# Performance work log

Hardware: AMD Instinct MI355X
Metric: run time of the kernel (lower is better)

Reference implementation:

```python
import jax, jax.numpy as jnp
import numpy as np

NE, S, B, IN, H, L, NL = 16, 16, 256, 61, 1024, 512, 2


def _gru_cell(x, h, wih, whh, bih, bhh):
    # PyTorch GRUCell math, gate order (r, z, n)
    gi = x @ wih.T + bih
    gh = h @ whh.T + bhh
    i_r, i_z, i_n = jnp.split(gi, 3, axis=-1)
    h_r, h_z, h_n = jnp.split(gh, 3, axis=-1)
    r = jax.nn.sigmoid(i_r + h_r)
    z = jax.nn.sigmoid(i_z + h_z)
    n = jnp.tanh(i_n + r * h_n)
    return (1.0 - z) * n + z * h


def setup_inputs():
    key = jax.random.key(0)
    ks = jax.random.split(key, 26)
    def w(i, shape, s=0.05):
        return jax.random.normal(ks[i], shape, jnp.float32) * s
    return {
        "target": jax.random.normal(ks[0], (NE * S, B, IN), jnp.float32),
        "latent": jax.random.normal(ks[1], (B, L), jnp.float32),
        "h0": jnp.zeros((NL, B, H), jnp.float32),
        "h0_dec": jax.random.normal(ks[2], (NE, NL, B, H), jnp.float32),
        "c_wih0": w(3, (3 * H, L)), "c_whh0": w(4, (3 * H, H)),
        "c_bih0": w(5, (3 * H,)), "c_bhh0": w(6, (3 * H,)),
        "c_wih1": w(7, (3 * H, H)), "c_whh1": w(8, (3 * H, H)),
        "c_bih1": w(9, (3 * H,)), "c_bhh1": w(10, (3 * H,)),
        "ce_w": w(11, (L, H)), "ce_b": w(12, (L,)),
        "d_wih0": w(13, (3 * H, IN + L)), "d_whh0": w(14, (3 * H, H)),
        "d_bih0": w(15, (3 * H,)), "d_bhh0": w(16, (3 * H,)),
        "d_wih1": w(17, (3 * H, H)), "d_whh1": w(18, (3 * H, H)),
        "d_bih1": w(19, (3 * H,)), "d_bhh1": w(20, (3 * H,)),
        "o_w": w(21, (IN, H)), "o_b": w(22, (IN,)),
    }


def reference(target, latent, h0, h0_dec,
              c_wih0, c_whh0, c_bih0, c_bhh0,
              c_wih1, c_whh1, c_bih1, c_bhh1,
              ce_w, ce_b,
              d_wih0, d_whh0, d_bih0, d_bhh0,
              d_wih1, d_whh1, d_bih1, d_bhh1,
              o_w, o_b):
    # --- Conductor: NE single-timestep 2-layer GRU steps, same latent input each step ---
    def cond_step(h, _):
        h0n = _gru_cell(latent, h[0], c_wih0, c_whh0, c_bih0, c_bhh0)
        h1n = _gru_cell(h0n, h[1], c_wih1, c_whh1, c_bih1, c_bhh1)
        return jnp.stack([h0n, h1n]), h1n
    _, c_out = jax.lax.scan(cond_step, h0, None, length=NE)  # [NE, B, H]
    emb = jnp.tanh(c_out @ ce_w.T + ce_b)                    # [NE, B, L]

    # --- Decoder (teacher forcing): segments independent -> fold NE into batch ---
    x = target.reshape(NE, S, B, IN).transpose(1, 0, 2, 3)   # [S, NE, B, IN]
    emb_rep = jnp.broadcast_to(emb[None], (S, NE, B, L))
    e = jnp.concatenate([x, emb_rep], axis=-1).reshape(S, NE * B, IN + L)
    hd = h0_dec.transpose(1, 0, 2, 3).reshape(NL, NE * B, H)

    def dec_step(h, xt):
        h0n = _gru_cell(xt, h[0], d_wih0, d_whh0, d_bih0, d_bhh0)
        h1n = _gru_cell(h0n, h[1], d_wih1, d_whh1, d_bih1, d_bhh1)
        return jnp.stack([h0n, h1n]), h1n
    _, y = jax.lax.scan(dec_step, hd, e)                     # [S, NE*B, H]

    probs = jax.nn.softmax(y @ o_w.T + o_b, axis=-1)         # [S, NE*B, IN]
    out = probs.reshape(S, NE, B, IN).transpose(1, 0, 2, 3).reshape(NE * S, B, IN)
    return out
```

## Files before the change

kernel.cpp:

```cpp
#include <hip/hip_runtime.h>
#include <hip/hip_bf16.h>
#include <cstdint>
#include <cstddef>

#define NEc 16
#define SSc 16
#define BBc 256
#define INc 61
#define HHc 1024
#define LLc 512
#define H3c 3072
#define NEBc 4096
#define KXc 64
#define HB  16

typedef __hip_bfloat16 bf16;
typedef __attribute__((ext_vector_type(8))) short bf16x8;
typedef __attribute__((ext_vector_type(4))) float f32x4;
typedef __attribute__((ext_vector_type(4))) short s16x4;

__device__ __forceinline__ void gload16(const void* g, void* l){
    __builtin_amdgcn_global_load_lds((const __attribute__((address_space(1))) unsigned int*)g,
                                     (__attribute__((address_space(3))) unsigned int*)l, 16, 0, 0);
}

__device__ __forceinline__ float sigmoidf_(float x){ return 1.0f/(1.0f+__expf(-x)); }

struct Slice {
    const bf16* A0; int lda0; int K0;
    const bf16* A1; int lda1; int K1;
    const bf16* A2; int lda2;
    const bf16* Wlo;
    const bf16* Whi;
    const float* bp;
    const float* hin;
    float* hout;
    bf16* hbout;
    bf16* out2;
    int mode;
};

#define GRU_KSTEP(APTR, ALDA, ACOL, BPTR, BLDB, BCOL, NIDX)                              \
  {                                                                                      \
    if (!first) __syncthreads();                                                         \
    first = false;                                                                       \
    _Pragma("unroll")                                                                    \
    for (int i=0;i<MR;i++){                                                              \
        const int o = i*4096 + tid*16;                                                   \
        const int u = o ^ (((o>>7)&7)<<4);                                               \
        gload16((APTR) + (size_t)(m0 + (u>>7))*(ALDA) + (ACOL) + ((u&127)>>1), sA + o);  \
    }                                                                                    \
    _Pragma("unroll")                                                                    \
    for (int i=0;i<6;i++){                                                               \
        const int o = i*4096 + tid*16;                                                   \
        const int u = o ^ (((o>>7)&7)<<4);                                               \
        gload16((BPTR) + (size_t)(u>>7)*(BLDB) + (BCOL) + ((u&127)>>1), sB + o);         \
    }                                                                                    \
    __syncthreads();                                                                     \
    _Pragma("unroll")                                                                    \
    for (int ks=0;ks<2;ks++){                                                            \
        bf16x8 av[MR];                                                                   \
        _Pragma("unroll")                                                                \
        for (int mi=0;mi<MR;mi++){                                                       \
            const int r = wm*(BM/2) + mi*16 + lr;                                        \
            const int u = r*128 + ks*64 + lk*16;                                         \
            av[mi] = *(const bf16x8*)(sA + (u ^ ((r&7)<<4)));                            \
        }                                                                                \
        _Pragma("unroll")                                                                \
        for (int hs=0;hs<2;hs++){                                                        \
            _Pragma("unroll")                                                            \
            for (int g3=0;g3<3;g3++){                                                    \
                const int br = ((wc*2+hs)*3 + g3)*16 + lr;                               \
                const int u  = br*128 + ks*64 + lk*16;                                   \
                const bf16x8 bv = *(const bf16x8*)(sB + (u ^ ((br&7)<<4)));              \
                const int gi_ = (g3<2) ? g3 : (NIDX);                                    \
                _Pragma("unroll")                                                        \
                for (int mi=0;mi<MR;mi++)                                                \
                    acc[mi][hs][gi_] = __builtin_amdgcn_mfma_f32_16x16x32_bf16(          \
                        av[mi], bv, acc[mi][hs][gi_], 0,0,0);                            \
            }                                                                            \
        }                                                                                \
    }                                                                                    \
  }

template<int BM>
__device__ void gru_body(const Slice& s, char* smem)
{
    constexpr int MR = BM/32;
    char* sA = smem;
    char* sB = smem + BM*128;

    const int tid  = threadIdx.x;
    const int lane = tid & 63;
    const int wave = tid >> 6;
    const int wm   = wave >> 1;
    const int wc   = wave & 1;
    const int lr   = lane & 15;
    const int lk   = lane >> 4;
    const int hb   = blockIdx.y;
    const int m0   = blockIdx.x * BM;

    const int Klo = s.K0 + s.K1;
    const bf16* WloB = s.Wlo + (size_t)hb*192*Klo;
    const bf16* WhiB = s.Whi + (size_t)hb*192*1024;

    f32x4 acc[MR][2][4];
    #pragma unroll
    for (int mi=0;mi<MR;mi++)
      #pragma unroll
      for (int hs=0;hs<2;hs++)
        #pragma unroll
        for (int g=0;g<4;g++)
          #pragma unroll
          for (int j=0;j<4;j++) acc[mi][hs][g][j] = 0.f;

    float hpre[2][MR][4];
    #pragma unroll
    for (int hs=0;hs<2;hs++)
      #pragma unroll
      for (int mi=0;mi<MR;mi++)
        #pragma unroll
        for (int j=0;j<4;j++){
            const int rl = wm*(BM/2) + mi*16 + lk*4 + j;
            hpre[hs][mi][j] = s.hin[(size_t)(m0+rl)*HHc + hb*64 + (wc*2+hs)*16 + lr];
        }

    bool first = true;

    {
        const bf16* Ap = s.A0; const int Al = s.lda0; const int Kp = s.K0;
        for (int k0 = 0; k0 < Kp; k0 += 64) GRU_KSTEP(Ap, Al, k0, WloB, Klo, k0, 2)
    }
    if (s.K1 > 0){
        const bf16* Ap = s.A1; const int Al = s.lda1; const int Kp = s.K1; const int c0 = s.K0;
        for (int k0 = 0; k0 < Kp; k0 += 64) GRU_KSTEP(Ap, Al, k0, WloB, Klo, c0 + k0, 2)
    }
    {
        const bf16* Ap = s.A2; const int Al = s.lda2;
        for (int k0 = 0; k0 < 1024; k0 += 64) GRU_KSTEP(Ap, Al, k0, WhiB, 1024, k0, 3)
    }

    #pragma unroll
    for (int hs=0;hs<2;hs++){
        const int hsub = wc*2 + hs;
        const int hc   = hb*64 + hsub*16 + lr;
        const float bpr  = s.bp[hb*256 +       hsub*16 + lr];
        const float bpz  = s.bp[hb*256 +  64 + hsub*16 + lr];
        const float bpin = s.bp[hb*256 + 128 + hsub*16 + lr];
        const float bphn = s.bp[hb*256 + 192 + hsub*16 + lr];
        #pragma unroll
        for (int mi=0;mi<MR;mi++)
          #pragma unroll
          for (int j=0;j<4;j++){
            const int rl = wm*(BM/2) + mi*16 + lk*4 + j;
            const int m  = m0 + rl;
            const float r = sigmoidf_(acc[mi][hs][0][j] + bpr);
            const float z = sigmoidf_(acc[mi][hs][1][j] + bpz);
            const float n = tanhf(acc[mi][hs][2][j] + bpin + r*(acc[mi][hs][3][j] + bphn));
            const size_t off = (size_t)m*HHc + hc;
            const float hnew = (1.f - z)*n + z*hpre[hs][mi][j];
            s.hout[off] = hnew;
            const bf16 hb16 = __float2bfloat16(hnew);
            s.hbout[off] = hb16;
            if (s.out2) s.out2[off] = hb16;
          }
    }
}

__device__ void owsm_body(const Slice& s, char* smem)
{
    if (blockIdx.y != 0) return;
    char* sA = smem; char* sB = smem + 8192;
    const int tid  = threadIdx.x;
    const int lane = tid & 63;
    const int wave = tid >> 6;
    const int wm   = wave >> 1;
    const int wc   = wave & 1;
    const int lr   = lane & 15;
    const int lk   = lane >> 4;
    const int m0   = blockIdx.x * 64;
    const int t    = s.K0;

    f32x4 acc[2][2];
    #pragma unroll
    for (int mi=0;mi<2;mi++)
      #pragma unroll
      for (int ni=0;ni<2;ni++)
        #pragma unroll
        for (int j=0;j<4;j++) acc[mi][ni][j]=0.f;

    for (int k0=0;k0<1024;k0+=64){
        if (k0) __syncthreads();
        #pragma unroll
        for (int i=0;i<2;i++){
            const int o = i*4096 + tid*16;
            const int u = o ^ (((o>>7)&7)<<4);
            gload16(s.A0 + (size_t)(m0 + (u>>7))*1024 + k0 + ((u&127)>>1), sA + o);
        }
        #pragma unroll
        for (int i=0;i<2;i++){
            const int o = i*4096 + tid*16;
            const int u = o ^ (((o>>7)&7)<<4);
            gload16(s.Wlo + (size_t)(u>>7)*1024 + k0 + ((u&127)>>1), sB + o);
        }
        __syncthreads();
        #pragma unroll
        for (int ks=0;ks<2;ks++){
            bf16x8 av[2], bv[2];
            #pragma unroll
            for (int mi=0;mi<2;mi++){
                const int r = wm*32 + mi*16 + lr;
                const int u = r*128 + ks*64 + lk*16;
                av[mi] = *(const bf16x8*)(sA + (u ^ ((r&7)<<4)));
            }
            #pragma unroll
            for (int ni=0;ni<2;ni++){
                const int r = wc*32 + ni*16 + lr;
                const int u = r*128 + ks*64 + lk*16;
                bv[ni] = *(const bf16x8*)(sB + (u ^ ((r&7)<<4)));
            }
            #pragma unroll
            for (int mi=0;mi<2;mi++)
              #pragma unroll
              for (int ni=0;ni<2;ni++)
                acc[mi][ni] = __builtin_amdgcn_mfma_f32_16x16x32_bf16(av[mi], bv[ni], acc[mi][ni], 0,0,0);
        }
    }
    __syncthreads();
    float* lg = (float*)smem;
    #pragma unroll
    for (int mi=0;mi<2;mi++)
      #pragma unroll
      for (int ni=0;ni<2;ni++)
        #pragma unroll
        for (int j=0;j<4;j++){
            const int rl = wm*32 + mi*16 + lk*4 + j;
            const int c  = wc*32 + ni*16 + lr;
            lg[rl*68 + c] = (c < INc) ? (acc[mi][ni][j] + s.bp[c]) : -1e30f;
        }
    __syncthreads();
    const int row = tid >> 2;
    const int q   = tid & 3;
    float mx = -1e30f;
    #pragma unroll
    for (int i=0;i<16;i++) mx = fmaxf(mx, lg[row*68 + q*16+i]);
    mx = fmaxf(mx, __shfl_xor(mx,1));
    mx = fmaxf(mx, __shfl_xor(mx,2));
    float ev[16];
    float sum = 0.f;
    #pragma unroll
    for (int i=0;i<16;i++){ ev[i] = __expf(lg[row*68 + q*16+i] - mx); sum += ev[i]; }
    sum += __shfl_xor(sum,1);
    sum += __shfl_xor(sum,2);
    const float inv = 1.f/sum;
    const int R = m0 + row;
    const int ne = R >> 8, b = R & 255;
    float* op = s.hout + ((size_t)((ne*SSc + t)*BBc + b))*INc;
    #pragma unroll
    for (int i=0;i<16;i++){
        const int c = q*16 + i;
        if (c < INc) op[c] = ev[i]*inv;
    }
}

template<int BM>
__global__ __launch_bounds__(256)
void fused_step(Slice s0, Slice s1, Slice s2)
{
    __shared__ char smem[(BM+192)*128];
    const Slice& s = (blockIdx.z==0) ? s0 : (blockIdx.z==1) ? s1 : s2;
    if (s.mode < 0) return;
    if constexpr (BM>=64){
        if (s.mode == 1){ owsm_body(s, smem); return; }
    }
    gru_body<BM>(s, smem);
}

template<int BM,int BN>
__global__ __launch_bounds__(256)
void gemm_bf(const bf16* __restrict__ A, const bf16* __restrict__ Bm, float* __restrict__ C,
             int K, int ldc)
{
    constexpr int WAVES_M = (BM==128) ? 2 : 1;
    constexpr int WM = BM / WAVES_M;
    constexpr int WN = BN / (4/WAVES_M);
    constexpr int MR = WM / 16;
    constexpr int NR = WN / 16;
    constexpr int ASW = (BM*128)/4096;
    constexpr int BSW = (BN*128)/4096;

    __shared__ char smem[(BM+BN)*128];
    char* sA = smem;
    char* sB = smem + BM*128;

    const int tid  = threadIdx.x;
    const int lane = tid & 63;
    const int wave = tid >> 6;
    const int wm   = (WAVES_M==2) ? (wave>>1) : 0;
    const int wn   = (WAVES_M==2) ? (wave&1)  : wave;
    const int lr   = lane & 15;
    const int lk   = lane >> 4;
    const int m0   = blockIdx.y * BM;
    const int n0   = blockIdx.x * BN;

    f32x4 acc[MR][NR];
    #pragma unroll
    for (int mi=0;mi<MR;mi++)
      #pragma unroll
      for (int ni=0;ni<NR;ni++)
        #pragma unroll
        for (int j=0;j<4;j++) acc[mi][ni][j] = 0.f;

    for (int k0 = 0; k0 < K; k0 += 64){
        if (k0) __syncthreads();
        #pragma unroll
        for (int i=0;i<ASW;i++){
            const int o = i*4096 + tid*16;
            const int u = o ^ (((o>>7)&7)<<4);
            gload16(A + (size_t)(m0 + (u>>7))*K + k0 + ((u&127)>>1), sA + o);
        }
        #pragma unroll
        for (int i=0;i<BSW;i++){
            const int o = i*4096 + tid*16;
            const int u = o ^ (((o>>7)&7)<<4);
            gload16(Bm + (size_t)(n0 + (u>>7))*K + k0 + ((u&127)>>1), sB + o);
        }
        __syncthreads();
        #pragma unroll
        for (int ks=0;ks<2;ks++){
            bf16x8 av[MR], bv[NR];
            #pragma unroll
            for (int mi=0;mi<MR;mi++){
                const int r = wm*WM + mi*16 + lr;
                const int u = r*128 + ks*64 + lk*16;
                av[mi] = *(const bf16x8*)(sA + (u ^ ((r&7)<<4)));
            }
            #pragma unroll
            for (int ni=0;ni<NR;ni++){
                const int r = wn*WN + ni*16 + lr;
                const int u = r*128 + ks*64 + lk*16;
                bv[ni] = *(const bf16x8*)(sB + (u ^ ((r&7)<<4)));
            }
            #pragma unroll
            for (int mi=0;mi<MR;mi++)
              #pragma unroll
              for (int ni=0;ni<NR;ni++)
                acc[mi][ni] = __builtin_amdgcn_mfma_f32_16x16x32_bf16(av[mi], bv[ni], acc[mi][ni], 0,0,0);
        }
    }
    #pragma unroll
    for (int mi=0;mi<MR;mi++)
      #pragma unroll
      for (int ni=0;ni<NR;ni++)
        #pragma unroll
        for (int j=0;j<4;j++){
            const int r = m0 + wm*WM + mi*16 + lk*4 + j;
            const int c = n0 + wn*WN + ni*16 + lr;
            C[(size_t)r*ldc + c] = acc[mi][ni][j];
        }
}

__global__ __launch_bounds__(256) void pack_w2(const float* __restrict__ src, int srcld,
                                               int col0, int Kvalid, int Kchunk,
                                               bf16* __restrict__ dst, int dstld, int dstc0,
                                               int total){
    const int idx = blockIdx.x*256 + threadIdx.x;
    if (idx >= total) return;
    const int k  = idx % Kchunk;
    const int c  = (idx / Kchunk) % 192;
    const int hb = idx / (Kchunk*192);
    const int g  = c >> 4;
    const int hsub = g/3;
    const int gate = g - hsub*3;
    const int row = gate*HHc + hb*64 + hsub*16 + (c & 15);
    const float v = (k < Kvalid) ? src[(size_t)row*srcld + col0 + k] : 0.f;
    dst[((size_t)hb*192 + c)*dstld + dstc0 + k] = __float2bfloat16(v);
}

__global__ __launch_bounds__(256) void pack_bias(const float* __restrict__ bih,
                                                 const float* __restrict__ bhh,
                                                 float* __restrict__ bp){
    const int idx = blockIdx.x*256 + threadIdx.x;
    if (idx >= HB*256) return;
    const int c  = idx & 255;
    const int hb = idx >> 8;
    const int i  = hb*64 + (c&63);
    const int g  = c >> 6;
    float v;
    if      (g==0) v = bih[i] + bhh[i];
    else if (g==1) v = bih[HHc+i] + bhh[HHc+i];
    else if (g==2) v = bih[2*HHc+i];
    else           v = bhh[2*HHc+i];
    bp[idx] = v;
}

__global__ __launch_bounds__(256) void cvt_bf16_k(const float* __restrict__ in, bf16* __restrict__ out, int n4){
    const int i = blockIdx.x*256 + threadIdx.x;
    if (i >= n4) return;
    const f32x4 v = *(const f32x4*)(in + (size_t)i*4);
    union { s16x4 s; bf16 b[4]; } u;
    #pragma unroll
    for (int j=0;j<4;j++) u.b[j] = __float2bfloat16(v[j]);
    *(s16x4*)(out + (size_t)i*4) = u.s;
}

__global__ __launch_bounds__(256) void pad_ow(const float* __restrict__ w, bf16* __restrict__ o){
    const int idx = blockIdx.x*256 + threadIdx.x;
    if (idx >= KXc*HHc) return;
    const int r = idx >> 10;
    o[idx] = __float2bfloat16(r < INc ? w[(size_t)r*HHc + (idx & (HHc-1))] : 0.f);
}

__global__ __launch_bounds__(256) void build_xb(const float* __restrict__ t, bf16* __restrict__ xb){
    const int idx = blockIdx.x*256 + threadIdx.x;
    if (idx >= SSc*NEBc*KXc) return;
    const int c  = idx & 63;
    const int rr = idx >> 6;
    const int s  = rr >> 12;
    const int r  = rr & 4095;
    const int ne = r >> 8;
    const int b  = r & 255;
    const float v = (c < INc) ? t[(((size_t)(ne*SSc + s)*BBc + b)*INc) + c] : 0.f;
    xb[idx] = __float2bfloat16(v);
}

__global__ __launch_bounds__(256) void init_hc(const float* __restrict__ h0,
                                               float* __restrict__ h0c, float* __restrict__ h1c,
                                               bf16* __restrict__ h0cb, bf16* __restrict__ h1cb){
    const int i = blockIdx.x*256 + threadIdx.x;
    if (i >= (BBc*HHc)/4) return;
    const int e = i*4;
    f32x4 a = *(const f32x4*)(h0 + e);
    f32x4 b = *(const f32x4*)(h0 + BBc*HHc + e);
    union { s16x4 v; bf16 q[4]; } ua, ub;
    #pragma unroll
    for (int j=0;j<4;j++){ ua.q[j]=__float2bfloat16(a[j]); ub.q[j]=__float2bfloat16(b[j]); }
    *(f32x4*)(h0c + e) = a; *(f32x4*)(h1c + e) = b;
    *(s16x4*)(h0cb + e) = ua.v; *(s16x4*)(h1cb + e) = ub.v;
}

__global__ __launch_bounds__(256) void init_hd(const float* __restrict__ hd,
                                               float* __restrict__ hd0, float* __restrict__ hd1,
                                               bf16* __restrict__ hd0b, bf16* __restrict__ hd1b){
    const int i = blockIdx.x*256 + threadIdx.x;
    if (i >= (NEBc*HHc)/4) return;
    const int e  = i*4;
    const int hh = e & (HHc-1);
    const int r  = e >> 10;
    const int ne = r >> 8;
    const int b  = r & 255;
    f32x4 a = *(const f32x4*)(hd + (((size_t)ne*2 + 0)*BBc + b)*HHc + hh);
    f32x4 c = *(const f32x4*)(hd + (((size_t)ne*2 + 1)*BBc + b)*HHc + hh);
    union { s16x4 v; bf16 q[4]; } ua, uc;
    #pragma unroll
    for (int j=0;j<4;j++){ ua.q[j]=__float2bfloat16(a[j]); uc.q[j]=__float2bfloat16(c[j]); }
    *(f32x4*)(hd0 + e) = a; *(f32x4*)(hd1 + e) = c;
    *(s16x4*)(hd0b + e) = ua.v; *(s16x4*)(hd1b + e) = uc.v;
}

__global__ __launch_bounds__(256) void bias_tanh4(const float* __restrict__ in,
                                                  const float* __restrict__ b, bf16* __restrict__ out){
    const int i = blockIdx.x*256 + threadIdx.x;
    if (i >= (NEBc*LLc)/4) return;
    const int e = i*4;
    const int c = e & (LLc-1);
    f32x4 v = *(const f32x4*)(in + e);
    f32x4 bb = *(const f32x4*)(b + c);
    union { s16x4 s; bf16 q[4]; } u;
    #pragma unroll
    for (int j=0;j<4;j++) u.q[j] = __float2bfloat16(tanhf(v[j] + bb[j]));
    *(s16x4*)(out + e) = u.s;
}


extern "C" void kernel_launch(void* const* d_in, const int* in_sizes, int n_in,
                              void* d_out, int out_size, void* d_ws, size_t ws_size,
                              hipStream_t stream)
{
    const float* target = (const float*)d_in[0];
    const float* latent = (const float*)d_in[1];
    const float* h0     = (const float*)d_in[2];
    const float* h0_dec = (const float*)d_in[3];
    const float* c_wih0 = (const float*)d_in[4];
    const float* c_whh0 = (const float*)d_in[5];
    const float* c_bih0 = (const float*)d_in[6];
    const float* c_bhh0 = (const float*)d_in[7];
    const float* c_wih1 = (const float*)d_in[8];
    const float* c_whh1 = (const float*)d_in[9];
    const float* c_bih1 = (const float*)d_in[10];
    const float* c_bhh1 = (const float*)d_in[11];
    const float* ce_w   = (const float*)d_in[12];
    const float* ce_b   = (const float*)d_in[13];
    const float* d_wih0 = (const float*)d_in[14];
    const float* d_whh0 = (const float*)d_in[15];
    const float* d_bih0 = (const float*)d_in[16];
    const float* d_bhh0 = (const float*)d_in[17];
    const float* d_wih1 = (const float*)d_in[18];
    const float* d_whh1 = (const float*)d_in[19];
    const float* d_bih1 = (const float*)d_in[20];
    const float* d_bhh1 = (const float*)d_in[21];
    const float* o_w    = (const float*)d_in[22];
    const float* o_b    = (const float*)d_in[23];
    float* out = (float*)d_out;

    float* fp = (float*)d_ws;
    auto fa = [&](size_t n){ float* q = fp; fp += n; return q; };
    float* hd0f[2] = { fa((size_t)NEBc*HHc), fa((size_t)NEBc*HHc) };
    float* hd1f[2] = { fa((size_t)NEBc*HHc), fa((size_t)NEBc*HHc) };
    float* h0cf[2] = { fa((size_t)BBc*HHc),  fa((size_t)BBc*HHc) };
    float* h1cf[2] = { fa((size_t)BBc*HHc),  fa((size_t)BBc*HHc) };
    float* emb   = fa((size_t)NEBc*LLc);
    float* bp_c0 = fa(HB*256);
    float* bp_c1 = fa(HB*256);
    float* bp_d0 = fa(HB*256);
    float* bp_d1 = fa(HB*256);

    bf16* bbp = (bf16*)fp;
    auto ba = [&](size_t n){ bf16* q = bbp; bbp += n; return q; };
    bf16* hd0b[2] = { ba((size_t)NEBc*HHc), ba((size_t)NEBc*HHc) };
    bf16* hd1b[2] = { ba((size_t)NEBc*HHc), ba((size_t)NEBc*HHc) };
    bf16* h0cb[2] = { ba((size_t)BBc*HHc),  ba((size_t)BBc*HHc) };
    bf16* h1cb[2] = { ba((size_t)BBc*HHc),  ba((size_t)BBc*HHc) };
    bf16* xb     = ba((size_t)SSc*NEBc*KXc);
    bf16* coutb  = ba((size_t)NEBc*HHc);
    bf16* embb   = ba((size_t)NEBc*LLc);
    bf16* latb   = ba((size_t)BBc*LLc);
    bf16* Wloc0  = ba((size_t)HB*192*LLc);
    bf16* Whic0  = ba((size_t)HB*192*HHc);
    bf16* Wloc1  = ba((size_t)HB*192*HHc);
    bf16* Whic1  = ba((size_t)HB*192*HHc);
    bf16* Wlod0f = ba((size_t)HB*192*576);
    bf16* Whid0  = ba((size_t)HB*192*HHc);
    bf16* Wlod1  = ba((size_t)HB*192*HHc);
    bf16* Whid1  = ba((size_t)HB*192*HHc);
    bf16* cewb   = ba((size_t)LLc*HHc);
    bf16* owb    = ba((size_t)KXc*HHc);

    auto packw = [&](const float* src, int srcld, int col0, int kv, int kchunk,
                     bf16* dst, int dstld, int dstc0){
        const int tot = HB*192*kchunk;
        hipLaunchKernelGGL(pack_w2, dim3((tot+255)/256), dim3(256),0,stream,
                           src,srcld,col0,kv,kchunk,dst,dstld,dstc0,tot);
    };

    hipLaunchKernelGGL(cvt_bf16_k, dim3((BBc*LLc/4+255)/256), dim3(256),0,stream, latent, latb, BBc*LLc/4);
    hipLaunchKernelGGL(cvt_bf16_k, dim3((LLc*HHc/4+255)/256), dim3(256),0,stream, ce_w, cewb, LLc*HHc/4);
    hipLaunchKernelGGL(pad_ow, dim3((KXc*HHc)/256), dim3(256),0,stream, o_w, owb);
    hipLaunchKernelGGL(build_xb, dim3((SSc*NEBc*KXc)/256), dim3(256),0,stream, target, xb);
    hipLaunchKernelGGL(init_hc, dim3((BBc*HHc/4)/256), dim3(256),0,stream, h0, h0cf[0], h1cf[0], h0cb[0], h1cb[0]);
    hipLaunchKernelGGL(init_hd, dim3((NEBc*HHc/4)/256), dim3(256),0,stream, h0_dec, hd0f[0], hd1f[0], hd0b[0], hd1b[0]);
    packw(c_wih0, LLc,     0,   LLc, LLc,  Wloc0, LLc, 0);
    packw(c_whh0, HHc,     0,   HHc, HHc,  Whic0, HHc, 0);
    packw(c_wih1, HHc,     0,   HHc, HHc,  Wloc1, HHc, 0);
    packw(c_whh1, HHc,     0,   HHc, HHc,  Whic1, HHc, 0);
    packw(d_wih0, INc+LLc, 0,   INc, KXc,  Wlod0f, 576, 0);
    packw(d_wih0, INc+LLc, INc, LLc, LLc,  Wlod0f, 576, KXc);
    packw(d_whh0, HHc,     0,   HHc, HHc,  Whid0, HHc, 0);
    packw(d_wih1, HHc,     0,   HHc, HHc,  Wlod1, HHc, 0);
    packw(d_whh1, HHc,     0,   HHc, HHc,  Whid1, HHc, 0);
    hipLaunchKernelGGL(pack_bias, dim3((HB*256+255)/256), dim3(256),0,stream, c_bih0, c_bhh0, bp_c0);
    hipLaunchKernelGGL(pack_bias, dim3((HB*256+255)/256), dim3(256),0,stream, c_bih1, c_bhh1, bp_c1);
    hipLaunchKernelGGL(pack_bias, dim3((HB*256+255)/256), dim3(256),0,stream, d_bih0, d_bhh0, bp_d0);
    hipLaunchKernelGGL(pack_bias, dim3((HB*256+255)/256), dim3(256),0,stream, d_bih1, d_bhh1, bp_d1);

    auto CL0 = [&](int s){ Slice x{}; x.mode=0;
        x.A0=latb; x.lda0=LLc; x.K0=LLc; x.A1=nullptr; x.lda1=0; x.K1=0;
        x.A2=h0cb[s&1]; x.lda2=HHc; x.Wlo=Wloc0; x.Whi=Whic0; x.bp=bp_c0;
        x.hin=h0cf[s&1]; x.hout=h0cf[(s+1)&1]; x.hbout=h0cb[(s+1)&1]; x.out2=nullptr; return x; };
    auto CL1 = [&](int s){ Slice x{}; x.mode=0;
        x.A0=h0cb[(s+1)&1]; x.lda0=HHc; x.K0=HHc; x.A1=nullptr; x.lda1=0; x.K1=0;
        x.A2=h1cb[s&1]; x.lda2=HHc; x.Wlo=Wloc1; x.Whi=Whic1; x.bp=bp_c1;
        x.hin=h1cf[s&1]; x.hout=h1cf[(s+1)&1]; x.hbout=h1cb[(s+1)&1];
        x.out2=coutb + (size_t)s*BBc*HHc; return x; };
    auto DL0 = [&](int t){ Slice x{}; x.mode=0;
        x.A0=xb + (size_t)t*NEBc*KXc; x.lda0=KXc; x.K0=KXc;
        x.A1=embb; x.lda1=LLc; x.K1=LLc;
        x.A2=hd0b[t&1]; x.lda2=HHc; x.Wlo=Wlod0f; x.Whi=Whid0; x.bp=bp_d0;
        x.hin=hd0f[t&1]; x.hout=hd0f[(t+1)&1]; x.hbout=hd0b[(t+1)&1]; x.out2=nullptr; return x; };
    auto DL1 = [&](int t){ Slice x{}; x.mode=0;
        x.A0=hd0b[(t+1)&1]; x.lda0=HHc; x.K0=HHc; x.A1=nullptr; x.lda1=0; x.K1=0;
        x.A2=hd1b[t&1]; x.lda2=HHc; x.Wlo=Wlod1; x.Whi=Whid1; x.bp=bp_d1;
        x.hin=hd1f[t&1]; x.hout=hd1f[(t+1)&1]; x.hbout=hd1b[(t+1)&1]; x.out2=nullptr; return x; };
    auto OW = [&](int t){ Slice x{}; x.mode=1;
        x.A0=hd1b[(t+1)&1]; x.K0=t; x.Wlo=owb; x.bp=o_b; x.hout=out; return x; };
    Slice NS{}; NS.mode = -1;

    hipLaunchKernelGGL((fused_step<32>), dim3(BBc/32, HB, 1), dim3(256),0,stream, CL0(0), NS, NS);
    for (int s=0;s<NEc;s++){
        if (s < NEc-1)
            hipLaunchKernelGGL((fused_step<32>), dim3(BBc/32, HB, 2), dim3(256),0,stream,
                               CL1(s), CL0(s+1), NS);
        else
            hipLaunchKernelGGL((fused_step<32>), dim3(BBc/32, HB, 1), dim3(256),0,stream,
                               CL1(s), NS, NS);
    }

    hipLaunchKernelGGL((gemm_bf<64,128>), dim3(LLc/128, NEBc/64), dim3(256),0,stream,
                       coutb, cewb, emb, HHc, LLc);
    hipLaunchKernelGGL(bias_tanh4, dim3((NEBc*LLc/4)/256), dim3(256),0,stream, emb, ce_b, embb);

    hipLaunchKernelGGL((fused_step<64>), dim3(NEBc/64, HB, 1), dim3(256),0,stream, DL0(0), NS, NS);
    for (int t=0;t<SSc;t++){
        Slice s1 = (t < SSc-1) ? DL0(t+1) : NS;
        Slice s2 = (t >= 1) ? OW(t-1) : NS;
        const int nz = (t >= 1) ? 3 : 2;
        hipLaunchKernelGGL((fused_step<64>), dim3(NEBc/64, HB, nz), dim3(256),0,stream,
                           DL1(t), s1, s2);
    }
    hipLaunchKernelGGL((fused_step<64>), dim3(NEBc/64, 1, 1), dim3(256),0,stream, OW(SSc-1), NS, NS);
}
```

Measured before the change: 2.993 ms.

## Pre-pack GRU weights into MFMA fragment layout and read directly from global

Weights are repacked so each wave's B-operand fragment for a 32-wide K window is a contiguous 512-element chunk indexed by lane. The kernel now reads weights straight from global/L2 into registers instead of staging them through LDS, which shrinks shared memory and removes the B tile global-to-LDS copy per K-step. The previous-hidden preload is also dropped and re-read at the epilogue. The risk is that register-level global loads of weights stall the MFMA stream, since they are not pipelined and sit on the critical path after the barrier.

```diff
diff --git a/kernel.cpp b/kernel.cpp
--- a/kernel.cpp
+++ b/kernel.cpp
@@ -40,21 +40,15 @@
     int mode;
 };
 
-#define GRU_KSTEP(APTR, ALDA, ACOL, BPTR, BLDB, BCOL, NIDX)                              \
+#define GRU_KSTEP(APTR, ALDA, ACOL, WF, KW, NIDX)                                        \
   {                                                                                      \
     if (!first) __syncthreads();                                                         \
     first = false;                                                                       \
     _Pragma("unroll")                                                                    \
-    for (int i=0;i<MR;i++){                                                              \
+    for (int i=0;i<ASW;i++){                                                             \
         const int o = i*4096 + tid*16;                                                   \
         const int u = o ^ (((o>>7)&7)<<4);                                               \
         gload16((APTR) + (size_t)(m0 + (u>>7))*(ALDA) + (ACOL) + ((u&127)>>1), sA + o);  \
-    }                                                                                    \
-    _Pragma("unroll")                                                                    \
-    for (int i=0;i<6;i++){                                                               \
-        const int o = i*4096 + tid*16;                                                   \
-        const int u = o ^ (((o>>7)&7)<<4);                                               \
-        gload16((BPTR) + (size_t)(u>>7)*(BLDB) + (BCOL) + ((u&127)>>1), sB + o);         \
     }                                                                                    \
     __syncthreads();                                                                     \
     _Pragma("unroll")                                                                    \
@@ -66,13 +60,13 @@
             const int u = r*128 + ks*64 + lk*16;                                         \
             av[mi] = *(const bf16x8*)(sA + (u ^ ((r&7)<<4)));                            \
         }                                                                                \
+        const bf16* wp = (WF) + ((size_t)((KW)+ks)*12)*512 + (size_t)lane*8;             \
         _Pragma("unroll")                                                                \
         for (int hs=0;hs<2;hs++){                                                        \
             _Pragma("unroll")                                                            \
             for (int g3=0;g3<3;g3++){                                                    \
-                const int br = ((wc*2+hs)*3 + g3)*16 + lr;                               \
-                const int u  = br*128 + ks*64 + lk*16;                                   \
-                const bf16x8 bv = *(const bf16x8*)(sB + (u ^ ((br&7)<<4)));              \
+                const int f = (wc*2+hs)*3 + g3;                                          \
+                const bf16x8 bv = *(const bf16x8*)(wp + f*512);                          \
                 const int gi_ = (g3<2) ? g3 : (NIDX);                                    \
                 _Pragma("unroll")                                                        \
                 for (int mi=0;mi<MR;mi++)                                                \
@@ -86,9 +80,9 @@
 template<int BM>
 __device__ void gru_body(const Slice& s, char* smem)
 {
-    constexpr int MR = BM/32;
+    constexpr int MR  = BM/32;
+    constexpr int ASW = (BM*128)/4096;
     char* sA = smem;
-    char* sB = smem + BM*128;
 
     const int tid  = threadIdx.x;
     const int lane = tid & 63;
@@ -101,8 +95,8 @@
     const int m0   = blockIdx.x * BM;
 
     const int Klo = s.K0 + s.K1;
-    const bf16* WloB = s.Wlo + (size_t)hb*192*Klo;
-    const bf16* WhiB = s.Whi + (size_t)hb*192*1024;
+    const bf16* WloF = s.Wlo + (size_t)hb * ((size_t)(Klo>>5)*12*512);
+    const bf16* WhiF = s.Whi + (size_t)hb * ((size_t)32*12*512);
 
     f32x4 acc[MR][2][4];
     #pragma unroll
@@ -114,30 +108,19 @@
           #pragma unroll
           for (int j=0;j<4;j++) acc[mi][hs][g][j] = 0.f;
 
-    float hpre[2][MR][4];
-    #pragma unroll
-    for (int hs=0;hs<2;hs++)
-      #pragma unroll
-      for (int mi=0;mi<MR;mi++)
-        #pragma unroll
-        for (int j=0;j<4;j++){
-            const int rl = wm*(BM/2) + mi*16 + lk*4 + j;
-            hpre[hs][mi][j] = s.hin[(size_t)(m0+rl)*HHc + hb*64 + (wc*2+hs)*16 + lr];
-        }
-
     bool first = true;
 
     {
         const bf16* Ap = s.A0; const int Al = s.lda0; const int Kp = s.K0;
-        for (int k0 = 0; k0 < Kp; k0 += 64) GRU_KSTEP(Ap, Al, k0, WloB, Klo, k0, 2)
+        for (int k0 = 0; k0 < Kp; k0 += 64) GRU_KSTEP(Ap, Al, k0, WloF, (k0>>5), 2)
     }
     if (s.K1 > 0){
         const bf16* Ap = s.A1; const int Al = s.lda1; const int Kp = s.K1; const int c0 = s.K0;
-        for (int k0 = 0; k0 < Kp; k0 += 64) GRU_KSTEP(Ap, Al, k0, WloB, Klo, c0 + k0, 2)
+        for (int k0 = 0; k0 < Kp; k0 += 64) GRU_KSTEP(Ap, Al, k0, WloF, ((c0+k0)>>5), 2)
     }
     {
         const bf16* Ap = s.A2; const int Al = s.lda2;
-        for (int k0 = 0; k0 < 1024; k0 += 64) GRU_KSTEP(Ap, Al, k0, WhiB, 1024, k0, 3)
+        for (int k0 = 0; k0 < 1024; k0 += 64) GRU_KSTEP(Ap, Al, k0, WhiF, (k0>>5), 3)
     }
 
     #pragma unroll
@@ -158,7 +141,7 @@
             const float z = sigmoidf_(acc[mi][hs][1][j] + bpz);
             const float n = tanhf(acc[mi][hs][2][j] + bpin + r*(acc[mi][hs][3][j] + bphn));
             const size_t off = (size_t)m*HHc + hc;
-            const float hnew = (1.f - z)*n + z*hpre[hs][mi][j];
+            const float hnew = (1.f - z)*n + z*s.hin[off];
             s.hout[off] = hnew;
             const bf16 hb16 = __float2bfloat16(hnew);
             s.hbout[off] = hb16;
@@ -267,7 +250,8 @@
 __global__ __launch_bounds__(256)
 void fused_step(Slice s0, Slice s1, Slice s2)
 {
-    __shared__ char smem[(BM+192)*128];
+    constexpr int SMEMSZ = (BM >= 64) ? 17408 : BM*128;
+    __shared__ char smem[SMEMSZ];
     const Slice& s = (blockIdx.z==0) ? s0 : (blockIdx.z==1) ? s1 : s2;
     if (s.mode < 0) return;
     if constexpr (BM>=64){
@@ -360,9 +344,9 @@
         }
 }
 
-__global__ __launch_bounds__(256) void pack_w2(const float* __restrict__ src, int srcld,
+__global__ __launch_bounds__(256) void pack_w3(const float* __restrict__ src, int srcld,
                                                int col0, int Kvalid, int Kchunk,
-                                               bf16* __restrict__ dst, int dstld, int dstc0,
+                                               bf16* __restrict__ dst, int nkw, int kw0,
                                                int total){
     const int idx = blockIdx.x*256 + threadIdx.x;
     if (idx >= total) return;
@@ -372,9 +356,13 @@
     const int g  = c >> 4;
     const int hsub = g/3;
     const int gate = g - hsub*3;
-    const int row = gate*HHc + hb*64 + hsub*16 + (c & 15);
-    const float v = (k < Kvalid) ? src[(size_t)row*srcld + col0 + k] : 0.f;
-    dst[((size_t)hb*192 + c)*dstld + dstc0 + k] = __float2bfloat16(v);
+    const int srow = gate*HHc + hb*64 + hsub*16 + (c & 15);
+    const float v = (k < Kvalid) ? src[(size_t)srow*srcld + col0 + k] : 0.f;
+    const int kwin = kw0 + (k >> 5);
+    const int kl   = k & 31;
+    const int lane = (kl >> 3)*16 + (c & 15);
+    const int j    = kl & 7;
+    dst[((((size_t)hb*nkw + kwin)*12 + g)*64 + lane)*8 + j] = __float2bfloat16(v);
 }
 
 __global__ __launch_bounds__(256) void pack_bias(const float* __restrict__ bih,
@@ -537,10 +525,10 @@
     bf16* owb    = ba((size_t)KXc*HHc);
 
     auto packw = [&](const float* src, int srcld, int col0, int kv, int kchunk,
-                     bf16* dst, int dstld, int dstc0){
+                     bf16* dst, int nkw, int kw0){
         const int tot = HB*192*kchunk;
-        hipLaunchKernelGGL(pack_w2, dim3((tot+255)/256), dim3(256),0,stream,
-                           src,srcld,col0,kv,kchunk,dst,dstld,dstc0,tot);
+        hipLaunchKernelGGL(pack_w3, dim3((tot+255)/256), dim3(256),0,stream,
+                           src,srcld,col0,kv,kchunk,dst,nkw,kw0,tot);
     };
 
     hipLaunchKernelGGL(cvt_bf16_k, dim3((BBc*LLc/4+255)/256), dim3(256),0,stream, latent, latb, BBc*LLc/4);
@@ -549,15 +537,15 @@
     hipLaunchKernelGGL(build_xb, dim3((SSc*NEBc*KXc)/256), dim3(256),0,stream, target, xb);
     hipLaunchKernelGGL(init_hc, dim3((BBc*HHc/4)/256), dim3(256),0,stream, h0, h0cf[0], h1cf[0], h0cb[0], h1cb[0]);
     hipLaunchKernelGGL(init_hd, dim3((NEBc*HHc/4)/256), dim3(256),0,stream, h0_dec, hd0f[0], hd1f[0], hd0b[0], hd1b[0]);
-    packw(c_wih0, LLc,     0,   LLc, LLc,  Wloc0, LLc, 0);
-    packw(c_whh0, HHc,     0,   HHc, HHc,  Whic0, HHc, 0);
-    packw(c_wih1, HHc,     0,   HHc, HHc,  Wloc1, HHc, 0);
-    packw(c_whh1, HHc,     0,   HHc, HHc,  Whic1, HHc, 0);
-    packw(d_wih0, INc+LLc, 0,   INc, KXc,  Wlod0f, 576, 0);
-    packw(d_wih0, INc+LLc, INc, LLc, LLc,  Wlod0f, 576, KXc);
-    packw(d_whh0, HHc,     0,   HHc, HHc,  Whid0, HHc, 0);
-    packw(d_wih1, HHc,     0,   HHc, HHc,  Wlod1, HHc, 0);
-    packw(d_whh1, HHc,     0,   HHc, HHc,  Whid1, HHc, 0);
+    packw(c_wih0, LLc,     0,   LLc, LLc, Wloc0, 16, 0);
+    packw(c_whh0, HHc,     0,   HHc, HHc, Whic0, 32, 0);
+    packw(c_wih1, HHc,     0,   HHc, HHc, Wloc1, 32, 0);
+    packw(c_whh1, HHc,     0,   HHc, HHc, Whic1, 32, 0);
+    packw(d_wih0, INc+LLc, 0,   INc, KXc, Wlod0f, 18, 0);
+    packw(d_wih0, INc+LLc, INc, LLc, LLc, Wlod0f, 18, 2);
+    packw(d_whh0, HHc,     0,   HHc, HHc, Whid0, 32, 0);
+    packw(d_wih1, HHc,     0,   HHc, HHc, Wlod1, 32, 0);
+    packw(d_whh1, HHc,     0,   HHc, HHc, Whid1, 32, 0);
     hipLaunchKernelGGL(pack_bias, dim3((HB*256+255)/256), dim3(256),0,stream, c_bih0, c_bhh0, bp_c0);
     hipLaunchKernelGGL(pack_bias, dim3((HB*256+255)/256), dim3(256),0,stream, c_bih1, c_bhh1, bp_c1);
     hipLaunchKernelGGL(pack_bias, dim3((HB*256+255)/256), dim3(256),0,stream, d_bih0, d_bhh0, bp_d0);
```

After: 4.246 ms. 1.42x slower.
